# Optimization experiments

Measured on AMD Instinct MI355X. Metric: run time of the kernel, lower is better.

The kernel has to match this reference:

```python
import jax, jax.numpy as jnp
import numpy as np

LAGRANGE_ORDER = 5  # fixed, as in the torch module


def _lagrange_weights(alpha):
    """Vectorised Lagrange weights of length L+1. alpha: [B,N] -> [B,N,L+1]."""
    L = LAGRANGE_ORDER
    j = jnp.arange(L + 1, dtype=alpha.dtype)
    u = alpha[..., None] - j                          # [B,N,L+1]
    denom = j[:, None] - j[None, :]                   # [L+1,L+1]
    mask = ~jnp.eye(L + 1, dtype=bool)
    num = jnp.where(mask, u[..., None, :], jnp.ones_like(u)[..., None, :])
    den = jnp.where(mask, denom, jnp.ones_like(denom))
    return (num / den).prod(axis=-1)                  # [B,N,L+1]


def setup_inputs() -> dict:
    key = jax.random.key(0)
    k1, k2, k3 = jax.random.split(key, 3)
    B, N = 16, 16384
    # fractional period in samples, in [40, 100) -> max floor(f0)=99, K=99+5+3=107<=108
    f0 = 40.0 + 60.0 * jax.random.uniform(k1, (B, N), dtype=jnp.float32)
    x = jax.random.normal(k2, (B, N), dtype=jnp.float32)
    l_b = jax.random.uniform(k3, (B, N, 2), dtype=jnp.float32)  # (g, p) in [0,1]
    return {"f0": f0, "x": x, "l_b": l_b, "K": 108}


def reference(f0, x, l_b, K):
    B, N = x.shape
    L = LAGRANGE_ORDER
    # design_loop: (g, p) -> loop taps [b0, a1]; gain capped <1 for stability
    g = 0.99 * l_b[..., 0]
    p = l_b[..., 1]
    b0 = g * (1.0 - p)                                # [B,N]
    a1 = g * p
    # tune_f0: subtract low-frequency phase delay of (b0 + a1 z^-1)
    f0c = f0 - a1 / (b0 + a1 + 1e-7)
    # Lagrange centre & weights
    z = jnp.floor(f0c).astype(jnp.int32)
    z_center = z - L // 2                             # [B,N]
    alpha = f0c - z_center.astype(f0.dtype)
    w = _lagrange_weights(alpha)                      # [B,N,L+1]
    # compute_resonator_matrix: loop filter convolved with fractional delay -> block [B,N,L+2]
    block = (b0[..., None] * jnp.pad(w, ((0, 0), (0, 0), (0, 1)))
             + a1[..., None] * jnp.pad(w, ((0, 0), (0, 0), (1, 0))))
    # scatter (-block) into A; LPC lag k+1 lives in column k
    cols = z_center[..., None] - 1 + jnp.arange(L + 2)  # [B,N,L+2]
    cols = jnp.clip(cols, 0, K - 1)
    A = jnp.zeros((B, N, K), x.dtype).at[
        jnp.arange(B)[:, None, None], jnp.arange(N)[None, :, None], cols
    ].add(-block)
    # sample_wise_lpc: y[n] = x[n] - sum_k A[n,k] * y[n-1-k], zero init state
    def step(buf, inp):
        a_n, x_n = inp                                 # [B,K], [B]
        y_n = x_n - jnp.sum(a_n * buf, axis=-1)
        buf = jnp.concatenate([y_n[:, None], buf[:, :-1]], axis=1)
        return buf, y_n
    buf0 = jnp.zeros((B, K), x.dtype)
    _, ys = jax.lax.scan(step, buf0, (A.transpose(1, 0, 2), x.T))  # ys: [N,B]
    return ys.T
```

## Files before the change

### kernel.cpp

```cpp
#include <hip/hip_runtime.h>
#include <math.h>


#define B_    16
#define N_    16384
#define S_    16
#define NSEG  1024
#define NITER 28
#define RUNS  104
#define CHUNK 37
#define RSTR  108

#define TG_FLOATS (B_ * S_ * RUNS * RUNS)
#define ST_FLOATS (B_ * S_ * RUNS)

__device__ __forceinline__ void diffks_coeffs(float f0v, float lbg, float lbp,
                                              int n, float4& lo, float4& hi) {
  float g  = 0.99f * lbg;
  float p  = lbp;
  float b0 = g * (1.0f - p);
  float a1 = g * p;
  float f0c = f0v - a1 / (b0 + a1 + 1e-7f);
  int   zc  = (int)floorf(f0c) - 2;
  float alpha = f0c - (float)zc;
  float u0 = alpha;
  float u1 = alpha - 1.0f;
  float u2 = alpha - 2.0f;
  float u3 = alpha - 3.0f;
  float u4 = alpha - 4.0f;
  float u5 = alpha - 5.0f;
  float w0 = u1 * u2 * u3 * u4 * u5 * (-1.0f / 120.0f);
  float w1 = u0 * u2 * u3 * u4 * u5 * ( 1.0f /  24.0f);
  float w2 = u0 * u1 * u3 * u4 * u5 * (-1.0f /  12.0f);
  float w3 = u0 * u1 * u2 * u4 * u5 * ( 1.0f /  12.0f);
  float w4 = u0 * u1 * u2 * u3 * u5 * (-1.0f /  24.0f);
  float w5 = u0 * u1 * u2 * u3 * u4 * ( 1.0f / 120.0f);
  lo.x = b0 * w0;
  lo.y = fmaf(b0, w1, a1 * w0);
  lo.z = fmaf(b0, w2, a1 * w1);
  lo.w = fmaf(b0, w3, a1 * w2);
  hi.x = fmaf(b0, w4, a1 * w3);
  hi.y = fmaf(b0, w5, a1 * w4);
  hi.z = a1 * w5;
  hi.w = __int_as_float((n - 6 - zc) & 255);
}

__global__ __launch_bounds__(832) void diffks_phase1(
    const float* __restrict__ f0, const float* __restrict__ lb,
    const float* __restrict__ x, float* __restrict__ Tg) {
  const int bs = blockIdx.x;
  const int b  = bs >> 4, s = bs & 15;
  const int n0 = s << 10;
  const int tid = threadIdx.x;

  __shared__ __align__(16) float hist[256 * RSTR];

  for (int i = tid; i < 64 * RSTR; i += 832)
    ((float4*)hist)[i] = float4{0.0f, 0.0f, 0.0f, 0.0f};
  __syncthreads();
  if (tid < 103) hist[(103 - tid) * RSTR + tid] = 1.0f;
  __syncthreads();

  const int w  = tid >> 6;
  const int ln = tid & 63;
  const int l  = ln & 31;
  const int h  = ln >> 5;
  const int c0 = 8 * w + 4 * h;
  const bool px = (w == 12) && (h == 1);

  const size_t gb = (size_t)b * N_ + n0;
  const float*  __restrict__ f0b = f0 + gb;
  const float2* __restrict__ lbb = (const float2*)(lb + 2 * gb);
  const float*  __restrict__ xb  = x + gb;

  float  nf0 = f0b[l];
  float2 nlb = lbb[l];
  float  nx  = xb[l];

  for (int t = 0; t < 32; ++t) {
    const int p = 32 * t + l;
    const float  cf0 = nf0;
    const float2 clb = nlb;
    const float  cx  = nx;
    if (t < 31) {
      nf0 = f0b[p + 32];
      nlb = lbb[p + 32];
      nx  = xb[p + 32];
    }
    float4 lo, hi;
    diffks_coeffs(cf0, clb.x, clb.y, p, lo, hi);
    const int base1 = (__float_as_int(hi.w) + 104) & 255;
    float4 acc;
    acc.x = 0.0f; acc.y = 0.0f; acc.z = 0.0f;
    acc.w = px ? cx : 0.0f;
    const float c[7] = {hi.z, hi.y, hi.x, lo.w, lo.z, lo.y, lo.x};
#pragma unroll
    for (int m = 0; m < 7; ++m) {
      const int row = (base1 + m) & 255;
      const float4 v = *(const float4*)&hist[row * RSTR + c0];
      acc.x = fmaf(c[m], v.x, acc.x);
      acc.y = fmaf(c[m], v.y, acc.y);
      acc.z = fmaf(c[m], v.z, acc.z);
      acc.w = fmaf(c[m], v.w, acc.w);
    }
    *(float4*)&hist[((p + 104) & 255) * RSTR + c0] = acc;
    __builtin_amdgcn_wave_barrier();
    asm volatile("" ::: "memory");
  }
  __syncthreads();

  float* __restrict__ T = Tg + (size_t)bs * RUNS * RUNS;
  for (int idx = tid; idx < RUNS * RUNS; idx += 832) {
    const int r = idx / RUNS;
    const int j = idx - r * RUNS;
    T[idx] = (j < 103) ? hist[((103 - j) & 255) * RSTR + r] : 0.0f;
  }
}

__global__ __launch_bounds__(832) void diffks_phase2(
    const float* __restrict__ Tg, float* __restrict__ states) {
  const int b   = blockIdx.x;
  const int tid = threadIdx.x;
  const int j   = tid % RUNS;
  const int q   = tid / RUNS;
  const int r0  = 13 * q;
  __shared__ float cur[RUNS];
  __shared__ float part[8][105];
  if (tid < 103) cur[tid] = 0.0f;
  if (tid == 103) cur[103] = 1.0f;
  __syncthreads();

  const float* __restrict__ Tb = Tg + (size_t)b * S_ * RUNS * RUNS;
  float tvA[13], tvB[13];
#pragma unroll
  for (int k = 0; k < 13; ++k) {
    tvA[k] = Tb[(size_t)(r0 + k) * RUNS + j];
    tvB[k] = Tb[(size_t)RUNS * RUNS + (size_t)(r0 + k) * RUNS + j];
  }

#pragma unroll
  for (int s = 0; s < S_; ++s) {
    float* tv = (s & 1) ? tvB : tvA;
    if (q == 0) states[((size_t)b * S_ + s) * RUNS + j] = cur[j];
    float acc = 0.0f;
#pragma unroll
    for (int k = 0; k < 13; ++k) acc = fmaf(tv[k], cur[r0 + k], acc);
    if (s + 2 < S_) {
      const float* __restrict__ Tn = Tb + (size_t)(s + 2) * RUNS * RUNS;
#pragma unroll
      for (int k = 0; k < 13; ++k)
        tv[k] = Tn[(size_t)(r0 + k) * RUNS + j];
    }
    part[q][j] = acc;
    __syncthreads();
    if (q == 0) {
      float v = 0.0f;
#pragma unroll
      for (int qq = 0; qq < 8; ++qq) v += part[qq][j];
      cur[j] = (j < 103) ? v : 1.0f;
    }
    __syncthreads();
  }
}

__global__ __launch_bounds__(256) void diffks_phase3(
    const float* __restrict__ f0, const float* __restrict__ lb,
    const float* __restrict__ x, const float* __restrict__ states,
    float* __restrict__ y) {
  const int bs = blockIdx.x;
  const int b  = bs >> 4, s = bs & 15;
  const int n0 = s << 10;
  const int tid = threadIdx.x;

  __shared__ __align__(16) float ring[512];
  __shared__ float4 sC[2 * NSEG];
  __shared__ float  sX[NSEG];
  __shared__ float  sY[NSEG];

  for (int i = tid; i < 512; i += 256) ring[i] = 0.0f;
  for (int i = tid; i < NSEG; i += 256) {
    const int n = n0 + i;
    const size_t gi = (size_t)b * N_ + n;
    float4 lo, hi;
    diffks_coeffs(f0[gi], lb[2 * gi], lb[2 * gi + 1], n, lo, hi);
    sC[2 * i] = lo; sC[2 * i + 1] = hi; sX[i] = x[gi];
  }
  __syncthreads();
  const float* __restrict__ st = states + (size_t)bs * RUNS;
  for (int k = tid; k < 103; k += 256) {
    const float v = st[k];
    ring[255 - k] = v;
    ring[511 - k] = v;
  }
  __syncthreads();

  if (tid < 64) {
    const int lane = tid;
    const bool act = (lane < CHUNK);
    for (int t = 0; t < NITER; ++t) {
      const int p = t * CHUNK + lane;
      if (act && p < NSEG) {
        const float4 lo = sC[2 * p];
        const float4 hi = sC[2 * p + 1];
        const float  xv = sX[p];
        const int base = __float_as_int(hi.w);
        const float r0 = ring[base + 0];
        const float r1 = ring[base + 1];
        const float r2 = ring[base + 2];
        const float r3 = ring[base + 3];
        const float r4 = ring[base + 4];
        const float r5 = ring[base + 5];
        const float r6 = ring[base + 6];
        const float s0 = fmaf(lo.x, r6, xv);
        const float s1 = fmaf(lo.y, r5, lo.z * r4);
        const float s2 = fmaf(lo.w, r3, hi.x * r2);
        const float s3 = fmaf(hi.y, r1, hi.z * r0);
        const float yv = (s0 + s1) + (s2 + s3);
        const int wsl = p & 255;
        ring[wsl]       = yv;
        ring[wsl + 256] = yv;
        sY[p] = yv;
      }
      __builtin_amdgcn_wave_barrier();
      asm volatile("" ::: "memory");
    }
  }
  __syncthreads();

  float4* __restrict__ yb = (float4*)(y + (size_t)b * N_ + n0);
  yb[tid] = ((const float4*)sY)[tid];
}

__global__ __launch_bounds__(256) void diffks_coeff_fb(
    const float* __restrict__ f0, const float* __restrict__ lb,
    float* __restrict__ cw, int total, int Nmask) {
  int idx = blockIdx.x * blockDim.x + threadIdx.x;
  if (idx >= total) return;
  float4 lo, hi;
  diffks_coeffs(f0[idx], lb[2 * idx], lb[2 * idx + 1], idx & Nmask, lo, hi);
  float4* out4 = (float4*)cw;
  out4[2 * idx]     = lo;
  out4[2 * idx + 1] = hi;
}

__global__ __launch_bounds__(64) void diffks_scan_fb(
    const float* __restrict__ x, const float* __restrict__ cw,
    float* __restrict__ y, int N) {
  const int b    = blockIdx.x;
  const int lane = threadIdx.x;
  __shared__ float ring[512];
#pragma unroll
  for (int i = 0; i < 8; ++i) ring[lane + 64 * i] = 0.0f;
  __builtin_amdgcn_wave_barrier();
  asm volatile("" ::: "memory");
  const float4* __restrict__ c4 = (const float4*)(cw + (size_t)b * N * 8);
  const float*  __restrict__ xb = x + (size_t)b * N;
  float*        __restrict__ yb = y + (size_t)b * N;
  const bool act = (lane < CHUNK);
  const int nIter = (N + CHUNK - 1) / CHUNK;
  for (int t = 0; t < nIter; ++t) {
    const int n = t * CHUNK + lane;
    if (act && n < N) {
      const float4 lo = c4[2 * n];
      const float4 hi = c4[2 * n + 1];
      const float  xv = xb[n];
      const int base = __float_as_int(hi.w);
      const float r0 = ring[base + 0];
      const float r1 = ring[base + 1];
      const float r2 = ring[base + 2];
      const float r3 = ring[base + 3];
      const float r4 = ring[base + 4];
      const float r5 = ring[base + 5];
      const float r6 = ring[base + 6];
      const float s0 = fmaf(lo.x, r6, xv);
      const float s1 = fmaf(lo.y, r5, lo.z * r4);
      const float s2 = fmaf(lo.w, r3, hi.x * r2);
      const float s3 = fmaf(hi.y, r1, hi.z * r0);
      const float yv = (s0 + s1) + (s2 + s3);
      ring[n & 255]         = yv;
      ring[(n & 255) + 256] = yv;
      yb[n] = yv;
    }
    __builtin_amdgcn_wave_barrier();
    asm volatile("" ::: "memory");
  }
}

extern "C" void kernel_launch(void* const* d_in, const int* in_sizes, int n_in,
                              void* d_out, int out_size, void* d_ws, size_t ws_size,
                              hipStream_t stream) {
  const float* f0 = (const float*)d_in[0];
  const float* x  = (const float*)d_in[1];
  const float* lb = (const float*)d_in[2];
  float* out = (float*)d_out;

  const int total = in_sizes[0];
  const size_t need = (size_t)(TG_FLOATS + ST_FLOATS) * 4;

  if (total == B_ * N_ && ws_size >= need) {
    float* Tg = (float*)d_ws;
    float* st = Tg + TG_FLOATS;
    diffks_phase1<<<B_ * S_, 832, 0, stream>>>(f0, lb, x, Tg);
    diffks_phase2<<<B_, 832, 0, stream>>>(Tg, st);
    diffks_phase3<<<B_ * S_, 256, 0, stream>>>(f0, lb, x, st, out);
  } else {
    const int N = total / B_;
    float* cw = (float*)d_ws;
    diffks_coeff_fb<<<(total + 255) / 256, 256, 0, stream>>>(f0, lb, cw, total, N - 1);
    diffks_scan_fb<<<B_, 64, 0, stream>>>(x, cw, out, N);
  }
}
```

Before: 112.5 us.

## Restructure phase1 to precompute coefficients in LDS and split timesteps across waves

Phase 1 now computes all 1024 segment coefficients and inputs up front, one per thread, and stores them in shared memory. The old code computed them inside the loop with register prefetch from global memory. The recurrence loop changes its work split: each of 16 waves now handles two timesteps per iteration across all 104 columns, two per lane. Before, each wave owned a fixed 8-column slice and its lanes walked through the timesteps. The block grows to 1024 threads, the history row stride drops to 104, and a block-wide __syncthreads per iteration replaces wave-local barriers, which adds synchronization cost and may change LDS bank-conflict behaviour.

```diff
diff --git a/kernel.cpp b/kernel.cpp
--- a/kernel.cpp
+++ b/kernel.cpp
@@ -9,7 +9,6 @@
 #define NITER 28
 #define RUNS  104
 #define CHUNK 37
-#define RSTR  108
 
 #define TG_FLOATS (B_ * S_ * RUNS * RUNS)
 #define ST_FLOATS (B_ * S_ * RUNS)
@@ -45,7 +44,7 @@
   hi.w = __int_as_float((n - 6 - zc) & 255);
 }
 
-__global__ __launch_bounds__(832) void diffks_phase1(
+__global__ __launch_bounds__(1024) void diffks_phase1(
     const float* __restrict__ f0, const float* __restrict__ lb,
     const float* __restrict__ x, float* __restrict__ Tg) {
   const int bs = blockIdx.x;
@@ -53,67 +52,59 @@
   const int n0 = s << 10;
   const int tid = threadIdx.x;
 
-  __shared__ __align__(16) float hist[256 * RSTR];
-
-  for (int i = tid; i < 64 * RSTR; i += 832)
+  __shared__ __align__(16) float hist[256 * RUNS];
+  __shared__ float4 sLo[NSEG], sHi[NSEG];
+  __shared__ float  sX[NSEG];
+
+  {
+    const size_t gi = (size_t)b * N_ + n0 + tid;
+    float4 lo, hi;
+    diffks_coeffs(f0[gi], lb[2 * gi], lb[2 * gi + 1], tid, lo, hi);
+    sLo[tid] = lo; sHi[tid] = hi; sX[tid] = x[gi];
+  }
+  for (int i = tid; i < 64 * RUNS; i += 1024)
     ((float4*)hist)[i] = float4{0.0f, 0.0f, 0.0f, 0.0f};
   __syncthreads();
-  if (tid < 103) hist[(103 - tid) * RSTR + tid] = 1.0f;
-  __syncthreads();
-
-  const int w  = tid >> 6;
-  const int ln = tid & 63;
-  const int l  = ln & 31;
-  const int h  = ln >> 5;
-  const int c0 = 8 * w + 4 * h;
-  const bool px = (w == 12) && (h == 1);
-
-  const size_t gb = (size_t)b * N_ + n0;
-  const float*  __restrict__ f0b = f0 + gb;
-  const float2* __restrict__ lbb = (const float2*)(lb + 2 * gb);
-  const float*  __restrict__ xb  = x + gb;
-
-  float  nf0 = f0b[l];
-  float2 nlb = lbb[l];
-  float  nx  = xb[l];
+  if (tid < 103) hist[(255 - tid) * RUNS + tid] = 1.0f;
+  __syncthreads();
+
+  const int w    = tid >> 6;
+  const int lane = tid & 63;
+  const int cl   = 2 * lane;
+  const bool act = (lane < 52);
+  const bool px  = (lane == 51);
 
   for (int t = 0; t < 32; ++t) {
-    const int p = 32 * t + l;
-    const float  cf0 = nf0;
-    const float2 clb = nlb;
-    const float  cx  = nx;
-    if (t < 31) {
-      nf0 = f0b[p + 32];
-      nlb = lbb[p + 32];
-      nx  = xb[p + 32];
-    }
-    float4 lo, hi;
-    diffks_coeffs(cf0, clb.x, clb.y, p, lo, hi);
-    const int base1 = (__float_as_int(hi.w) + 104) & 255;
-    float4 acc;
-    acc.x = 0.0f; acc.y = 0.0f; acc.z = 0.0f;
-    acc.w = px ? cx : 0.0f;
-    const float c[7] = {hi.z, hi.y, hi.x, lo.w, lo.z, lo.y, lo.x};
-#pragma unroll
-    for (int m = 0; m < 7; ++m) {
-      const int row = (base1 + m) & 255;
-      const float4 v = *(const float4*)&hist[row * RSTR + c0];
-      acc.x = fmaf(c[m], v.x, acc.x);
-      acc.y = fmaf(c[m], v.y, acc.y);
-      acc.z = fmaf(c[m], v.z, acc.z);
-      acc.w = fmaf(c[m], v.w, acc.w);
-    }
-    *(float4*)&hist[((p + 104) & 255) * RSTR + c0] = acc;
-    __builtin_amdgcn_wave_barrier();
-    asm volatile("" ::: "memory");
-  }
-  __syncthreads();
+#pragma unroll
+    for (int u = 0; u < 2; ++u) {
+      const int p = 32 * t + 2 * w + u;
+      const float4 lo = sLo[p];
+      const float4 hi = sHi[p];
+      const float  xv = sX[p];
+      if (act) {
+        const int base = __float_as_int(hi.w);
+        float2 acc;
+        acc.x = 0.0f;
+        acc.y = px ? xv : 0.0f;
+        const float c[7] = {hi.z, hi.y, hi.x, lo.w, lo.z, lo.y, lo.x};
+#pragma unroll
+        for (int m = 0; m < 7; ++m) {
+          const int row = (base + m) & 255;
+          const float2 v = *(const float2*)&hist[row * RUNS + cl];
+          acc.x = fmaf(c[m], v.x, acc.x);
+          acc.y = fmaf(c[m], v.y, acc.y);
+        }
+        *(float2*)&hist[(p & 255) * RUNS + cl] = acc;
+      }
+    }
+    __syncthreads();
+  }
 
   float* __restrict__ T = Tg + (size_t)bs * RUNS * RUNS;
-  for (int idx = tid; idx < RUNS * RUNS; idx += 832) {
+  for (int idx = tid; idx < RUNS * RUNS; idx += 1024) {
     const int r = idx / RUNS;
     const int j = idx - r * RUNS;
-    T[idx] = (j < 103) ? hist[((103 - j) & 255) * RSTR + r] : 0.0f;
+    T[idx] = (j < 103) ? hist[((255 - j) & 255) * RUNS + r] : 0.0f;
   }
 }
 
@@ -300,7 +291,7 @@
   if (total == B_ * N_ && ws_size >= need) {
     float* Tg = (float*)d_ws;
     float* st = Tg + TG_FLOATS;
-    diffks_phase1<<<B_ * S_, 832, 0, stream>>>(f0, lb, x, Tg);
+    diffks_phase1<<<B_ * S_, 1024, 0, stream>>>(f0, lb, x, Tg);
     diffks_phase2<<<B_, 832, 0, stream>>>(Tg, st);
     diffks_phase3<<<B_ * S_, 256, 0, stream>>>(f0, lb, x, st, out);
   } else {
```

After: 105.8 us. -5.9%, faster.
